# Kernel tuning notes

Hardware: AMD Instinct MI355X
Metric: run time of the kernel (lower is better)

Reference implementation:

```python
import jax, jax.numpy as jnp
import numpy as np

K = 2  # diffusion order
N, S, D, L, C = 4000, 32, 128, 2, 10
THETA = 0.5


def setup_inputs() -> dict:
    key = jax.random.key(0)
    ks = jax.random.split(key, 16)
    w = 0.05  # weight scale to keep tanh/exp in sane range
    return {
        "A": jax.random.uniform(ks[0], (N, N), dtype=jnp.float32),
        "embs": jax.random.normal(ks[1], (L, S, N, D), dtype=jnp.float32),
        "conv1_w": jax.random.normal(ks[2], (K, D, D), dtype=jnp.float32) * w,
        "conv2_w": jax.random.normal(ks[3], (K, D, D), dtype=jnp.float32) * w,
        "lin_in_w": jax.random.normal(ks[4], (D, D), dtype=jnp.float32) * w,
        "lin_out_w": jax.random.normal(ks[5], (D, 2 * D), dtype=jnp.float32) * w,
        "W_psi": jax.random.normal(ks[6], (2 * D, D), dtype=jnp.float32) * w,
        "b_psi": jax.random.normal(ks[7], (D,), dtype=jnp.float32) * w,
        "ae": jax.random.uniform(ks[8], (N, 1, 1), dtype=jnp.float32),
        "ab": jax.random.uniform(ks[9], (N, 1, 1), dtype=jnp.float32),
        "emb_table": jax.random.uniform(ks[10], (N, D), minval=-0.1, maxval=0.1, dtype=jnp.float32),
        "W_p": jax.random.normal(ks[11], (D, C), dtype=jnp.float32) * w,
        "W_c": jax.random.normal(ks[12], (D, D), dtype=jnp.float32) * w,
    }


def _diffusion(A_tilde, X, W):
    # A_tilde: [N,N] (sym-normalized); X: [N,S,D] (linear in X, so batching over S
    # is identical to the per-timestep loop); W: [K,D,D]
    P_f = A_tilde / A_tilde.sum(axis=1, keepdims=True)
    P_v = A_tilde.T / A_tilde.sum(axis=0, keepdims=True)
    Z = jnp.einsum('mn,nsd->msd', P_f, X) @ W[0]
    P_psi_f, P_psi_v = P_f, P_v
    for k in range(1, K):
        if k < K // 2:
            P_psi_f = P_psi_f @ P_f
            M = P_psi_f
        else:
            P_psi_v = P_psi_v @ P_v
            M = P_psi_v
        Z = Z + jnp.einsum('mn,nsd->msd', M, X) @ W[k]
    return Z


def _attention(context, lin_in_w, lin_out_w, ae, ab):
    # context: [N,S,D]; query is the last timestep, output_len == 1
    q = context[:, -1, :] @ lin_in_w.T                    # [N,D]
    scores = jnp.einsum('nd,nsd->ns', q, context)         # [N,S]
    attw = jax.nn.softmax(scores, axis=-1)                # [N,S]
    mix = attw[:, None, :] * context.transpose(0, 2, 1)   # [N,D,S]
    delta_t = jnp.arange(S - 1, -1, -1, dtype=context.dtype)  # flipped arange
    bt = jnp.exp(-ab * delta_t[None, None, :])            # [N,1,S]
    term2 = jax.nn.relu(ae * mix * bt)                    # [N,D,S]
    mix_sum = (term2 + mix).sum(axis=-1)                  # [N,D]
    combined = jnp.concatenate([mix_sum, q], axis=-1)     # [N,2D]
    return jnp.tanh(combined @ lin_out_w.T)               # [N,D]


def reference(A, embs, conv1_w, conv2_w, lin_in_w, lin_out_w, W_psi, b_psi,
              ae, ab, emb_table, W_p, W_c):
    n = A.shape[0]
    A_t = A + jnp.eye(n, dtype=A.dtype)
    d_inv_sqrt = A_t.sum(axis=1) ** -0.5
    A_tilde = d_inv_sqrt[:, None] * A_t * d_inv_sqrt[None, :]

    outs = []
    for l in range(L):
        X = embs[l].transpose(1, 0, 2)                    # [N,S,D]
        h = _diffusion(A_tilde, X, conv1_w)
        h = jax.nn.relu(h)
        h = _diffusion(A_tilde, h, conv2_w)               # [N,S,D]
        # fusion with theta = 0.5 (h_tilde is the raw embedding)
        fused = jnp.concatenate([THETA * h, (1.0 - THETA) * X], axis=-1) @ W_psi + b_psi
        outs.append(_attention(fused, lin_in_w, lin_out_w, ae, ab))
    outputs = jnp.stack(outs)                             # [L,N,D]

    # embedding lookup over arange(N) is an identity gather
    qs = jax.nn.relu(emb_table)                           # [N,D]
    betas = jnp.exp(jnp.einsum('nd,lne->lde', qs, jnp.tanh(outputs)))  # [L,D,D]
    betas = betas / betas.sum(axis=0)
    Z = jnp.einsum('lnd,lde->ne', outputs, betas)         # [N,D]

    P = jax.nn.softmax(Z @ W_p, axis=1)                   # [N,C]
    C_mat = P.T @ Z                                       # [C,D]
    eta = P.T @ A @ P                                     # [C,C] (vectorized eta_ij)
    C_prime = jax.nn.relu(eta @ (C_mat @ W_c.T))          # [C,D]
    return P @ C_prime                                    # [N,D]
```

## Files before the change

### kernel.cpp

```cpp
#include <hip/hip_runtime.h>
#include <hip/hip_bf16.h>


typedef __attribute__((ext_vector_type(8))) short short8;
typedef __attribute__((ext_vector_type(4))) float f32x4;
typedef __attribute__((ext_vector_type(4))) unsigned short us4;

__device__ __forceinline__ unsigned short f2bf(float x) {
  unsigned int u = __builtin_bit_cast(unsigned int, x);
  u += 0x7FFFu + ((u >> 16) & 1u);
  return (unsigned short)(u >> 16);
}

__device__ __forceinline__ void gload16(const void* g, void* l) {
  __builtin_amdgcn_global_load_lds((const __attribute__((address_space(1))) void*)g,
                                   (__attribute__((address_space(3))) void*)l, 16, 0, 0);
}

__device__ __forceinline__ void barrier_() {
  __builtin_amdgcn_sched_barrier(0);
  asm volatile("" ::: "memory");
  __builtin_amdgcn_s_barrier();
  asm volatile("" ::: "memory");
  __builtin_amdgcn_sched_barrier(0);
}

template<int TRANS, int RELU>
__global__ __launch_bounds__(512, 2)
void gemm256(const unsigned short* __restrict__ Ap, int lda,
             const unsigned short* __restrict__ Bp, int ldb,
             unsigned short* __restrict__ outp, int ldo, int K)
{
  __shared__ alignas(16) unsigned short lds[81920];
  const int t = threadIdx.x;
  const int lane = t & 63;
  const int wave = t >> 6;
  const int wm = wave >> 2;
  const int wn = wave & 3;
  const int lrow = lane & 15;
  const int kgrp = lane >> 4;
  const int slotbase = (kgrp ^ (lrow & 7)) << 3;

  const int b = blockIdx.x;
  const int wg = (b & 7) * 32 + (b >> 3);
  const int m0 = (wg >> 4) << 8;
  const int j0 = (wg & 15) << 8;

  const int prow = t >> 3;
  const int lslot = (t & 7) ^ (prow & 7);
  const unsigned short* srcA = Ap + (size_t)(m0 + prow) * lda + lslot * 8;
  const unsigned short* srcB = Bp + (size_t)(j0 + prow) * ldb + lslot * 8;
  const size_t a64 = (size_t)64 * lda, a128 = (size_t)128 * lda;
  const size_t b64 = (size_t)64 * ldb, b128 = (size_t)128 * ldb;
  unsigned short* dA = &lds[t * 8];
  unsigned short* dB = &lds[32768 + t * 8];
  const int NT = K >> 6;

#define STG_A(h, kb, kt) { const unsigned short* s_ = srcA + (h)*a128 + (size_t)(kt)*64; \
    gload16(s_, dA + (kb)*16384 + (h)*8192); \
    gload16(s_ + a64, dA + (kb)*16384 + (h)*8192 + 4096); }
#define STG_B(h, bb, kt) { const unsigned short* s_ = srcB + (h)*b128 + (size_t)(kt)*64; \
    gload16(s_, dB + (bb)*16384 + (h)*8192); \
    gload16(s_ + b64, dB + (bb)*16384 + (h)*8192 + 4096); }

  const int arb = wm * 8192 + lrow * 64 + slotbase;
  const int brb = (wn >> 1) * 8192 + ((wn & 1) << 12) + lrow * 64 + slotbase;

#define RD_A(dst, base_off) \
  _Pragma("unroll") for (int mf_ = 0; mf_ < 4; ++mf_) { \
    dst[mf_][0] = *(const short8*)&lds[(base_off) + mf_*1024]; \
    dst[mf_][1] = *(const short8*)&lds[((base_off) ^ 32) + mf_*1024]; }
#define RD_B(dst, base_off) \
  _Pragma("unroll") for (int nf_ = 0; nf_ < 2; ++nf_) { \
    dst[nf_][0] = *(const short8*)&lds[(base_off) + nf_*1024]; \
    dst[nf_][1] = *(const short8*)&lds[((base_off) ^ 32) + nf_*1024]; }

#define MFMA16(AF, BF, MB, NB) \
  _Pragma("unroll") for (int mf_ = 0; mf_ < 4; ++mf_) \
  _Pragma("unroll") for (int nf_ = 0; nf_ < 2; ++nf_) { \
    acc[(MB)+mf_][(NB)+nf_] = __builtin_amdgcn_mfma_f32_16x16x32_bf16(AF[mf_][0], BF[nf_][0], acc[(MB)+mf_][(NB)+nf_], 0,0,0); \
    acc[(MB)+mf_][(NB)+nf_] = __builtin_amdgcn_mfma_f32_16x16x32_bf16(AF[mf_][1], BF[nf_][1], acc[(MB)+mf_][(NB)+nf_], 0,0,0); }

#define LGKM(n) { asm volatile("s_waitcnt lgkmcnt(" #n ")" ::: "memory"); \
                  __builtin_amdgcn_sched_barrier(0); }

  f32x4 acc[8][4];
#pragma unroll
  for (int i = 0; i < 8; ++i)
#pragma unroll
    for (int j = 0; j < 4; ++j) acc[i][j] = f32x4{0.f, 0.f, 0.f, 0.f};

  short8 a0[4][2], a1[4][2], b0[2][2], b1[2][2];

  STG_B(0, 0, 0); STG_B(1, 0, 0); STG_A(0, 0, 0); STG_A(1, 0, 0);
  STG_B(0, 1, 1); STG_B(1, 1, 1); STG_A(0, 1, 1); STG_A(1, 1, 1);
  asm volatile("s_waitcnt vmcnt(8)" ::: "memory");
  barrier_();
  RD_A(a0, arb);
  RD_B(b0, 32768 + brb);

  int rb3 = 0, rn3 = 1, sb3 = 2;
  for (int V = 0; V < NT; ++V) {
    const int abuf  = (V & 1) << 14;
    const int anbuf = ((V + 1) & 1) << 14;
    const int bbuf  = 32768 + (rb3 << 14);
    const int bnbuf = 32768 + (rn3 << 14);
    const bool stg = (V + 2 < NT);
    const bool rdn = (V + 1 < NT);

    RD_B(b1, bbuf + brb + 2048);
    LGKM(4);
    if (stg) STG_B(0, sb3, V + 2);
    __builtin_amdgcn_s_setprio(1);
    MFMA16(a0, b0, 0, 0);
    __builtin_amdgcn_s_setprio(0);
    barrier_();

    RD_A(a1, abuf + arb + 4096);
    LGKM(8);
    if (stg) STG_B(1, sb3, V + 2);
    __builtin_amdgcn_s_setprio(1);
    MFMA16(a0, b1, 0, 2);
    __builtin_amdgcn_s_setprio(0);
    if (stg) { asm volatile("s_waitcnt vmcnt(4)" ::: "memory"); }
    else     { asm volatile("s_waitcnt vmcnt(0)" ::: "memory"); }
    barrier_();

    if (rdn) { RD_A(a0, anbuf + arb); LGKM(8); }
    else     { LGKM(0); }
    if (stg) STG_A(0, (V & 1), V + 2);
    __builtin_amdgcn_s_setprio(1);
    MFMA16(a1, b0, 4, 0);
    __builtin_amdgcn_s_setprio(0);
    barrier_();

    if (rdn) { RD_B(b0, bnbuf + brb); LGKM(4); }
    else     { LGKM(0); }
    if (stg) STG_A(1, (V & 1), V + 2);
    __builtin_amdgcn_s_setprio(1);
    MFMA16(a1, b1, 4, 2);
    __builtin_amdgcn_s_setprio(0);
    barrier_();

    rb3 = rn3; rn3 = (rn3 == 2) ? 0 : rn3 + 1;
    sb3 = (sb3 == 2) ? 0 : sb3 + 1;
  }

#pragma unroll
  for (int mf = 0; mf < 8; ++mf) {
#pragma unroll
    for (int nf = 0; nf < 4; ++nf) {
      const int m = m0 + wm * 128 + mf * 16 + kgrp * 4;
      const int j = j0 + wn * 64 + nf * 16 + lrow;
      if (TRANS) {
        us4 pk;
#pragma unroll
        for (int r = 0; r < 4; ++r) pk[r] = f2bf(acc[mf][nf][r]);
        *(us4*)(outp + (size_t)j * ldo + m) = pk;
      } else {
#pragma unroll
        for (int r = 0; r < 4; ++r) {
          float v = acc[mf][nf][r];
          if (RELU) v = fmaxf(v, 0.f);
          outp[(size_t)(m + r) * ldo + j] = f2bf(v);
        }
      }
    }
  }
#undef STG_A
#undef STG_B
#undef RD_A
#undef RD_B
#undef MFMA16
#undef LGKM
}

template<int EPI, int RELU, int BIAS>
__global__ __launch_bounds__(256)
void gemm_nt(const unsigned short* __restrict__ A1,
             const unsigned short* __restrict__ A2,
             int k_switch, int a_zstride, int lda,
             const unsigned short* __restrict__ B, int ldb,
             void* __restrict__ outp,
             long o_j, long o_m, long o_z, long o_jt,
             const float* __restrict__ bias, int K)
{
  __shared__ alignas(16) unsigned short At[128*32];
  __shared__ alignas(16) unsigned short Bt[128*32];
  const int t = threadIdx.x;
  const int lane = t & 63;
  const int wave = t >> 6;
  const int m0 = blockIdx.x << 7;
  const int jt = blockIdx.y;
  const int j0 = jt << 7;
  const int z  = blockIdx.z;
  const int wm = (wave >> 1) << 6;
  const int wn = (wave & 1) << 6;
  const int lrow = lane & 15;
  const int kgrp = lane >> 4;

  const unsigned short* A1z = A1 + (long)z * a_zstride;
  const unsigned short* A2z = A2 + (long)z * a_zstride;

  f32x4 acc[4][4];
#pragma unroll
  for (int i = 0; i < 4; ++i)
#pragma unroll
    for (int j = 0; j < 4; ++j) acc[i][j] = f32x4{0.f, 0.f, 0.f, 0.f};

  const int r0 = t >> 2, q0 = t & 3;
  const int c1 = t + 256;
  const int r1 = c1 >> 2, q1 = c1 & 3;

  for (int k0 = 0; k0 < K; k0 += 32) {
    const unsigned short* As; int ka;
    if (k0 < k_switch) { As = A1z; ka = k0; } else { As = A2z; ka = k0 - k_switch; }
    gload16(As + (long)(m0 + r0) * lda + ka + q0 * 8, At + t * 8);
    gload16(As + (long)(m0 + r1) * lda + ka + q1 * 8, At + c1 * 8);
    gload16(B  + (long)(j0 + r0) * ldb + k0 + q0 * 8, Bt + t * 8);
    gload16(B  + (long)(j0 + r1) * ldb + k0 + q1 * 8, Bt + c1 * 8);
    __syncthreads();
    short8 af[4], bv[4];
#pragma unroll
    for (int i = 0; i < 4; ++i)
      af[i] = *(const short8*)(At + (wm + i * 16 + lrow) * 32 + kgrp * 8);
#pragma unroll
    for (int i = 0; i < 4; ++i)
      bv[i] = *(const short8*)(Bt + (wn + i * 16 + lrow) * 32 + kgrp * 8);
#pragma unroll
    for (int i = 0; i < 4; ++i)
#pragma unroll
      for (int j = 0; j < 4; ++j)
        acc[i][j] = __builtin_amdgcn_mfma_f32_16x16x32_bf16(af[i], bv[j], acc[i][j], 0, 0, 0);
    __syncthreads();
  }

  const int mlb = wm + kgrp * 4;
#pragma unroll
  for (int i = 0; i < 4; ++i) {
#pragma unroll
    for (int j = 0; j < 4; ++j) {
      const int jl = wn + j * 16 + lrow;
      const int ml = mlb + i * 16;
      if (EPI == 0) {
        long base = (long)jl * o_j + (long)(m0 + ml) * o_m + (long)z * o_z + (long)jt * o_jt;
        us4 pk;
#pragma unroll
        for (int r = 0; r < 4; ++r) pk[r] = f2bf(acc[i][j][r]);
        *(us4*)((unsigned short*)outp + base) = pk;
      } else {
        float* of = (float*)outp;
        float badd = BIAS ? bias[j0 + jl] : 0.f;
#pragma unroll
        for (int r = 0; r < 4; ++r) {
          long idx = (long)jl * o_j + (long)(m0 + ml + r) * o_m + (long)z * o_z + (long)jt * o_jt;
          of[idx] = acc[i][j][r] + badd;
        }
      }
    }
  }
}

__global__ __launch_bounds__(256) void rowsum_dis(const float* __restrict__ A,
                                                  float* __restrict__ dis) {
  int m = blockIdx.x;
  if (m >= 4000) { if (threadIdx.x == 0) dis[m] = 0.f; return; }
  const float* r = A + (long)m * 4000;
  float a = 0.f;
  for (int i = threadIdx.x; i < 1000; i += 256) {
    float4 v = ((const float4*)r)[i];
    a += v.x + v.y + v.z + v.w;
  }
  for (int o = 32; o; o >>= 1) a += __shfl_xor(a, o);
  __shared__ float ls[4];
  if ((threadIdx.x & 63) == 0) ls[threadIdx.x >> 6] = a;
  __syncthreads();
  if (threadIdx.x == 0) dis[m] = rsqrtf(1.f + ls[0] + ls[1] + ls[2] + ls[3]);
}

__global__ __launch_bounds__(256) void wrow_kernel(const float* __restrict__ A,
                                                   const float* __restrict__ dis,
                                                   float* __restrict__ iwrow) {
  int m = blockIdx.x;
  if (m >= 4000) { if (threadIdx.x == 0) iwrow[m] = 0.f; return; }
  const float* r = A + (long)m * 4000;
  float a = 0.f;
  for (int n = threadIdx.x; n < 4000; n += 256) a += r[n] * dis[n];
  for (int o = 32; o; o >>= 1) a += __shfl_xor(a, o);
  __shared__ float ls[4];
  if ((threadIdx.x & 63) == 0) ls[threadIdx.x >> 6] = a;
  __syncthreads();
  if (threadIdx.x == 0) iwrow[m] = 1.f / (ls[0] + ls[1] + ls[2] + ls[3] + dis[m]);
}

__global__ __launch_bounds__(256) void wcol_part(const float* __restrict__ A,
                                                 const float* __restrict__ dis,
                                                 float* __restrict__ part) {
  int j = blockIdx.x * 256 + threadIdx.x;
  int mz = blockIdx.y;
  float a = 0.f;
  if (j < 4000) {
    int ms = mz * 125;
    for (int m = ms; m < ms + 125; ++m) a += A[(long)m * 4000 + j] * dis[m];
  }
  part[(long)mz * 4096 + j] = a;
}

__global__ __launch_bounds__(256) void wcol_fin(const float* __restrict__ part,
                                                const float* __restrict__ dis,
                                                float* __restrict__ iwcol) {
  int j = blockIdx.x * 256 + threadIdx.x;
  float s = 0.f;
  for (int z = 0; z < 32; ++z) s += part[(long)z * 4096 + j];
  iwcol[j] = (j < 4000) ? 1.f / (s + dis[j]) : 0.f;
}

__global__ __launch_bounds__(256) void build_P(const float* __restrict__ A,
                                               const float* __restrict__ dis,
                                               const float* __restrict__ iwrow,
                                               const float* __restrict__ iwcol,
                                               unsigned short* __restrict__ Pcat,
                                               unsigned short* __restrict__ PV,
                                               unsigned short* __restrict__ PVT) {
  __shared__ float tile[64][65];
  int m0 = blockIdx.y * 64, n0 = blockIdx.x * 64;
#pragma unroll
  for (int i = 0; i < 16; ++i) {
    int idx = i * 256 + threadIdx.x;
    int lr = idx >> 6, lc = idx & 63;
    int m = m0 + lr, n = n0 + lc;
    float v = 0.f;
    if (m < 4000 && n < 4000) {
      float a = A[(long)m * 4000 + n];
      if (m == n) a += 1.f;
      v = a * dis[n];
    }
    Pcat[(long)m * 8192 + n] = f2bf(v * iwrow[m]);
    float pv = v * iwcol[m];
    PVT[(long)m * 4096 + n] = f2bf(pv);
    tile[lr][lc] = pv;
  }
  __syncthreads();
#pragma unroll
  for (int i = 0; i < 16; ++i) {
    int idx = i * 256 + threadIdx.x;
    int lr = idx >> 6, lc = idx & 63;
    PV[(long)(n0 + lr) * 4096 + (m0 + lc)] = f2bf(tile[lc][lr]);
  }
}

__global__ __launch_bounds__(256) void prep_weights(const float* __restrict__ lin_in,
                                                    const float* __restrict__ lin_out,
                                                    const float* __restrict__ c1,
                                                    const float* __restrict__ c2,
                                                    const float* __restrict__ wpsi,
                                                    float* __restrict__ LWiT, float* __restrict__ LWoT,
                                                    unsigned short* __restrict__ CW1T,
                                                    unsigned short* __restrict__ CW2T,
                                                    unsigned short* __restrict__ WPST) {
  int i = blockIdx.x * 256 + threadIdx.x;
  if (i < 16384) {
    int e = i >> 7, d = i & 127;
    LWiT[e * 128 + d] = lin_in[d * 128 + e];
  } else if (i < 49152) {
    int k = i - 16384; int ii = k >> 7, d = k & 127;
    LWoT[k] = lin_out[d * 256 + ii];
  } else if (i < 81920) {
    int k = i - 49152; int j = k >> 7, kk = k & 127;
    CW1T[k] = f2bf(c1[(j >> 7) * 16384 + kk * 128 + (j & 127)]);
  } else if (i < 114688) {
    int k = i - 81920; int j = k >> 7, kk = k & 127;
    CW2T[k] = f2bf(c2[(j >> 7) * 16384 + kk * 128 + (j & 127)]);
  } else if (i < 147456) {
    int k = i - 114688; int e = k >> 8, d2 = k & 255;
    WPST[k] = f2bf(0.5f * wpsi[d2 * 128 + e]);
  }
}

__global__ __launch_bounds__(256) void convert_X(const float* __restrict__ embsL,
                                                 unsigned short* __restrict__ X) {
  long i4 = (long)blockIdx.x * 256 + threadIdx.x;
  long e = i4 << 2;
  int n = (int)(e >> 12);
  int r = (int)(e & 4095);
  us4 o;
  if (n < 4000) {
    int s = r >> 7, d = r & 127;
    float4 v = *(const float4*)(embsL + ((long)s * 4000 + n) * 128 + d);
    o[0] = f2bf(v.x); o[1] = f2bf(v.y); o[2] = f2bf(v.z); o[3] = f2bf(v.w);
  } else { o[0] = o[1] = o[2] = o[3] = 0; }
  *(us4*)(X + (long)n * 4096 + r) = o;
}

__global__ __launch_bounds__(128) void attention_kernel(const float* __restrict__ F,
                                                        const float* __restrict__ LWiT,
                                                        const float* __restrict__ LWoT,
                                                        const float* __restrict__ ae,
                                                        const float* __restrict__ ab,
                                                        float* __restrict__ outp) {
  int n = blockIdx.x, t = threadIdx.x;
  __shared__ float Fs[32 * 132];
  __shared__ float qv[128], msum[128], attw[32], btv[32];
  const float* Fr = F + (long)n * 4096;
  for (int i = t; i < 4096; i += 128) { int s = i >> 7, d = i & 127; Fs[s * 132 + d] = Fr[i]; }
  __syncthreads();
  {
    float a = 0.f;
    const float* Frow = Fs + 31 * 132;
    for (int e = 0; e < 128; ++e) a += Frow[e] * LWiT[e * 128 + t];
    qv[t] = a;
  }
  __syncthreads();
  if (t < 32) {
    float sc = 0.f;
    for (int d = 0; d < 128; ++d) sc += qv[d] * Fs[t * 132 + d];
    float mx = sc;
    for (int o = 16; o; o >>= 1) mx = fmaxf(mx, __shfl_xor(mx, o, 32));
    float ex = expf(sc - mx), sm = ex;
    for (int o = 16; o; o >>= 1) sm += __shfl_xor(sm, o, 32);
    attw[t] = ex / sm;
  } else if (t >= 64 && t < 96) {
    int s = t - 64;
    btv[s] = expf(-ab[n] * (float)(31 - s));
  }
  __syncthreads();
  {
    float aen = ae[n], acc = 0.f;
    for (int s = 0; s < 32; ++s) {
      float f = Fs[s * 132 + t];
      acc += attw[s] * (f + aen * btv[s] * fmaxf(f, 0.f));
    }
    msum[t] = acc;
  }
  __syncthreads();
  {
    float a = 0.f;
    for (int e = 0; e < 128; ++e) a += msum[e] * LWoT[e * 128 + t];
    for (int e = 0; e < 128; ++e) a += qv[e] * LWoT[(e + 128) * 128 + t];
    outp[(long)n * 128 + t] = tanhf(a);
  }
}

__global__ __launch_bounds__(256) void tanh_qs(const float* __restrict__ outs,
                                               const float* __restrict__ embt,
                                               float* __restrict__ T, float* __restrict__ qs) {
  long i = (long)blockIdx.x * 256 + threadIdx.x;
  if (i < 1024000) T[i] = tanhf(outs[i]);
  else { long j = i - 1024000; if (j < 512000) qs[j] = fmaxf(embt[j], 0.f); }
}

__global__ __launch_bounds__(256) void betas_raw_kernel(const float* __restrict__ qs,
                                                        const float* __restrict__ T,
                                                        float* __restrict__ braw) {
  int e = threadIdx.x & 127, dl = threadIdx.x >> 7;
  int d = blockIdx.x * 2 + dl, l = blockIdx.y;
  const float* Tl = T + (long)l * 512000;
  float acc = 0.f;
  for (int n = 0; n < 4000; ++n) acc += qs[(long)n * 128 + d] * Tl[(long)n * 128 + e];
  braw[((long)l * 128 + d) * 128 + e] = acc;
}

__global__ __launch_bounds__(256) void bnorm_kernel(const float* __restrict__ braw,
                                                    float* __restrict__ bn) {
  int i = blockIdx.x * 256 + threadIdx.x;
  float b0 = expf(braw[i]), b1 = expf(braw[16384 + i]);
  float s = b0 + b1;
  bn[i] = b0 / s;
  bn[16384 + i] = b1 / s;
}

__global__ __launch_bounds__(256) void z_kernel(const float* __restrict__ outs,
                                                const float* __restrict__ bn,
                                                float* __restrict__ Zb) {
  int n = blockIdx.x * 2 + (threadIdx.x >> 7);
  int e = threadIdx.x & 127;
  float acc = 0.f;
  for (int l = 0; l < 2; ++l) {
    const float* orow = outs + ((long)l * 4000 + n) * 128;
    const float* brow = bn + (long)l * 16384;
    for (int d = 0; d < 128; ++d) acc += orow[d] * brow[d * 128 + e];
  }
  Zb[(long)n * 128 + e] = acc;
}

__global__ __launch_bounds__(256) void p_kernel(const float* __restrict__ Zb,
                                                const float* __restrict__ Wp,
                                                float* __restrict__ P) {
  int n = blockIdx.x * 4 + (threadIdx.x >> 6);
  int c = threadIdx.x & 63;
  float val = 0.f;
  if (c < 10) {
    const float* zr = Zb + (long)n * 128;
    for (int d = 0; d < 128; ++d) val += zr[d] * Wp[d * 10 + c];
  }
  float mx = val;
  for (int i = 0; i < 10; ++i) mx = fmaxf(mx, __shfl(val, i, 64));
  float ex = (c < 10) ? expf(val - mx) : 0.f;
  float sm = 0.f;
  for (int i = 0; i < 10; ++i) sm += __shfl(ex, i, 64);
  if (c < 12) P[(long)n * 12 + c] = (c < 10) ? ex / sm : 0.f;
}

__global__ __launch_bounds__(256) void ap_kernel(const float* __restrict__ A,
                                                 const float* __restrict__ P,
                                                 float* __restrict__ AP) {
  int m = blockIdx.x, t = threadIdx.x;
  const float* Ar = A + (long)m * 4000;
  float acc[10];
#pragma unroll
  for (int c = 0; c < 10; ++c) acc[c] = 0.f;
  for (int n = t; n < 4000; n += 256) {
    float a = Ar[n];
    const float* Pr = P + (long)n * 12;
#pragma unroll
    for (int c = 0; c < 10; ++c) acc[c] += a * Pr[c];
  }
#pragma unroll
  for (int c = 0; c < 10; ++c)
    for (int o = 32; o; o >>= 1) acc[c] += __shfl_xor(acc[c], o);
  __shared__ float ls[4][10];
  if ((t & 63) == 0)
    for (int c = 0; c < 10; ++c) ls[t >> 6][c] = acc[c];
  __syncthreads();
  if (t < 10) AP[(long)m * 12 + t] = ls[0][t] + ls[1][t] + ls[2][t] + ls[3][t];
  if (t >= 10 && t < 12) AP[(long)m * 12 + t] = 0.f;
}

__global__ __launch_bounds__(256) void etacm_part(const float* __restrict__ P,
                                                  const float* __restrict__ AP,
                                                  const float* __restrict__ Z,
                                                  float* __restrict__ peta,
                                                  float* __restrict__ pcm) {
  int b = blockIdx.x, t = threadIdx.x;
  int ms = b * 63, me = ms + 63; if (me > 4000) me = 4000;
  int i_ = t / 10, j_ = t % 10;
  float ea = 0.f;
  float ca[5];
#pragma unroll
  for (int k = 0; k < 5; ++k) ca[k] = 0.f;
  for (int m = ms; m < me; ++m) {
    if (t < 100) ea += P[(long)m * 12 + i_] * AP[(long)m * 12 + j_];
#pragma unroll
    for (int k = 0; k < 5; ++k) {
      int idx = t + 256 * k;
      int c = idx >> 7, e = idx & 127;
      ca[k] += P[(long)m * 12 + c] * Z[(long)m * 128 + e];
    }
  }
  if (t < 100) peta[(long)b * 100 + t] = ea;
#pragma unroll
  for (int k = 0; k < 5; ++k) pcm[(long)b * 1280 + t + 256 * k] = ca[k];
}

__global__ __launch_bounds__(256) void final_small(const float* __restrict__ peta,
                                                   const float* __restrict__ pcm,
                                                   const float* __restrict__ Wc,
                                                   float* __restrict__ cprime) {
  __shared__ float eta_s[100], cm_s[1280], tmp_s[1280];
  int t = threadIdx.x;
  if (t < 100) {
    float s = 0.f;
    for (int b = 0; b < 64; ++b) s += peta[(long)b * 100 + t];
    eta_s[t] = s;
  }
  for (int i = t; i < 1280; i += 256) {
    float s = 0.f;
    for (int b = 0; b < 64; ++b) s += pcm[(long)b * 1280 + i];
    cm_s[i] = s;
  }
  __syncthreads();
  for (int i = t; i < 1280; i += 256) {
    int c = i >> 7, d = i & 127;
    float s = 0.f;
    for (int e = 0; e < 128; ++e) s += cm_s[c * 128 + e] * Wc[d * 128 + e];
    tmp_s[i] = s;
  }
  __syncthreads();
  for (int i = t; i < 1280; i += 256) {
    int c = i >> 7, d = i & 127;
    float s = 0.f;
    for (int j = 0; j < 10; ++j) s += eta_s[c * 10 + j] * tmp_s[j * 128 + d];
    cprime[i] = fmaxf(s, 0.f);
  }
}

__global__ __launch_bounds__(256) void out_kernel(const float* __restrict__ P,
                                                  const float* __restrict__ cpr,
                                                  float* __restrict__ out) {
  int idx = blockIdx.x * 256 + threadIdx.x;
  int n = idx >> 7, d = idx & 127;
  float s = 0.f;
#pragma unroll
  for (int c = 0; c < 10; ++c) s += P[(long)n * 12 + c] * cpr[c * 128 + d];
  out[idx] = s;
}

extern "C" void kernel_launch(void* const* d_in, const int* in_sizes, int n_in,
                              void* d_out, int out_size, void* d_ws, size_t ws_size,
                              hipStream_t stream) {
  (void)in_sizes; (void)n_in; (void)out_size; (void)ws_size;
  const float* A      = (const float*)d_in[0];
  const float* embs   = (const float*)d_in[1];
  const float* conv1w = (const float*)d_in[2];
  const float* conv2w = (const float*)d_in[3];
  const float* lin_in = (const float*)d_in[4];
  const float* lin_out= (const float*)d_in[5];
  const float* Wpsi   = (const float*)d_in[6];
  const float* bpsi   = (const float*)d_in[7];
  const float* ae     = (const float*)d_in[8];
  const float* ab     = (const float*)d_in[9];
  const float* embt   = (const float*)d_in[10];
  const float* Wp     = (const float*)d_in[11];
  const float* Wc     = (const float*)d_in[12];
  float* out = (float*)d_out;
  char* ws = (char*)d_ws;

  size_t off = 0;
  auto alloc = [&](size_t b) { size_t r = off; off += (b + 255) & ~(size_t)255; return r; };
  unsigned short* PCAT = (unsigned short*)(ws + alloc((size_t)4096 * 8192 * 2));
  char*           BTF  = ws + alloc((size_t)4096 * 8192 * 2);
  unsigned short* BT   = (unsigned short*)BTF;
  float*          Ff   = (float*)BTF;
  unsigned short* XBF  = (unsigned short*)(ws + alloc((size_t)4096 * 4096 * 2));
  unsigned short* PV   = XBF;
  unsigned short* HBUF = (unsigned short*)(ws + alloc((size_t)4096 * 4096 * 2));
  unsigned short* PVT  = HBUF;
  float* DIS   = (float*)(ws + alloc(4096 * 4));
  float* IWROW = (float*)(ws + alloc(4096 * 4));
  float* IWCOL = (float*)(ws + alloc(4096 * 4));
  float* WCP   = (float*)(ws + alloc((size_t)32 * 4096 * 4));
  float* LWIT  = (float*)(ws + alloc(16384 * 4));
  float* LWOT  = (float*)(ws + alloc(32768 * 4));
  unsigned short* CW1T = (unsigned short*)(ws + alloc(32768 * 2));
  unsigned short* CW2T = (unsigned short*)(ws + alloc(32768 * 2));
  unsigned short* WPST = (unsigned short*)(ws + alloc(32768 * 2));
  float* OUTS = (float*)(ws + alloc((size_t)2 * 4000 * 128 * 4));
  float* TT   = (float*)(ws + alloc((size_t)2 * 4000 * 128 * 4));
  float* QS   = (float*)(ws + alloc((size_t)4000 * 128 * 4));
  float* BRAW = (float*)(ws + alloc(32768 * 4));
  float* BNRM = (float*)(ws + alloc(32768 * 4));
  float* ZB   = (float*)(ws + alloc((size_t)4000 * 128 * 4));
  float* PP   = (float*)(ws + alloc((size_t)4000 * 12 * 4));
  float* APB  = (float*)(ws + alloc((size_t)4000 * 12 * 4));
  float* PETA = (float*)(ws + alloc((size_t)64 * 100 * 4));
  float* PCM  = (float*)(ws + alloc((size_t)64 * 1280 * 4));
  float* CPR  = (float*)(ws + alloc(1280 * 4));

  const int BIG = 1 << 30;

  rowsum_dis<<<4096, 256, 0, stream>>>(A, DIS);
  wrow_kernel<<<4096, 256, 0, stream>>>(A, DIS, IWROW);
  wcol_part<<<dim3(16, 32), 256, 0, stream>>>(A, DIS, WCP);
  wcol_fin<<<16, 256, 0, stream>>>(WCP, DIS, IWCOL);
  prep_weights<<<576, 256, 0, stream>>>(lin_in, lin_out, conv1w, conv2w, Wpsi,
                                        LWIT, LWOT, CW1T, CW2T, WPST);
  build_P<<<dim3(64, 64), 256, 0, stream>>>(A, DIS, IWROW, IWCOL, PCAT, PV, PVT);

  gemm256<1, 0><<<256, 512, 0, stream>>>(PVT, 4096, PV, 4096, PCAT + 4096, 8192, 4096);

  for (int l = 0; l < 2; ++l) {
    convert_X<<<16384, 256, 0, stream>>>(embs + (long)l * 32 * 4000 * 128, XBF);
    gemm_nt<0, 0, 0><<<dim3(32, 2, 32), 256, 0, stream>>>(
        XBF, XBF, BIG, 128, 4096, CW1T, 128,
        BT, 8192L, 1L, 128L * 8192, 4096L, nullptr, 128);
    gemm256<0, 1><<<256, 512, 0, stream>>>(PCAT, 8192, BT, 8192, HBUF, 4096, 8192);
    gemm_nt<0, 0, 0><<<dim3(32, 2, 32), 256, 0, stream>>>(
        HBUF, HBUF, BIG, 128, 4096, CW2T, 128,
        BT, 8192L, 1L, 128L * 8192, 4096L, nullptr, 128);
    gemm256<0, 0><<<256, 512, 0, stream>>>(PCAT, 8192, BT, 8192, HBUF, 4096, 8192);
    gemm_nt<2, 0, 1><<<dim3(32, 1, 32), 256, 0, stream>>>(
        HBUF, XBF, 128, 128, 4096, WPST, 256,
        Ff, 1L, 4096L, 128L, 0L, bpsi, 256);
    attention_kernel<<<4000, 128, 0, stream>>>(Ff, LWIT, LWOT, ae, ab,
                                               OUTS + (long)l * 512000);
  }

  tanh_qs<<<6000, 256, 0, stream>>>(OUTS, embt, TT, QS);
  betas_raw_kernel<<<dim3(64, 2), 256, 0, stream>>>(QS, TT, BRAW);
  bnorm_kernel<<<64, 256, 0, stream>>>(BRAW, BNRM);
  z_kernel<<<2000, 256, 0, stream>>>(OUTS, BNRM, ZB);
  p_kernel<<<1000, 256, 0, stream>>>(ZB, Wp, PP);
  ap_kernel<<<4000, 256, 0, stream>>>(A, PP, APB);
  etacm_part<<<64, 256, 0, stream>>>(PP, APB, ZB, PETA, PCM);
  final_small<<<1, 256, 0, stream>>>(PETA, PCM, Wc, CPR);
  out_kernel<<<2000, 256, 0, stream>>>(PP, CPR, out);
}
```

Measured before the change: 1.544 ms.

## Fold query projection into fused GEMM, batch attention output GEMM, split betas reduction

```diff
diff --git a/kernel.cpp b/kernel.cpp
--- a/kernel.cpp
+++ b/kernel.cpp
@@ -10,6 +10,10 @@
   unsigned int u = __builtin_bit_cast(unsigned int, x);
   u += 0x7FFFu + ((u >> 16) & 1u);
   return (unsigned short)(u >> 16);
+}
+__device__ __forceinline__ float bf2f(unsigned short u) {
+  unsigned int x = ((unsigned int)u) << 16;
+  return __builtin_bit_cast(float, x);
 }
 
 __device__ __forceinline__ void gload16(const void* g, void* l) {
@@ -175,18 +179,18 @@
 #undef LGKM
 }
 
-template<int EPI, int RELU, int BIAS>
-__global__ __launch_bounds__(256)
-void gemm_nt(const unsigned short* __restrict__ A1,
-             const unsigned short* __restrict__ A2,
-             int k_switch, int a_zstride, int lda,
-             const unsigned short* __restrict__ B, int ldb,
-             void* __restrict__ outp,
-             long o_j, long o_m, long o_z, long o_jt,
-             const float* __restrict__ bias, int K)
+template<int EPI, int KFULL, int MINB>
+__global__ __launch_bounds__(256, MINB)
+void gemm_smallk(const unsigned short* __restrict__ A1,
+                 const unsigned short* __restrict__ A2,
+                 int k_switch, int a_zstride, int lda,
+                 const unsigned short* __restrict__ B, int ldb,
+                 void* __restrict__ outp,
+                 long o_j, long o_m, long o_z, long o_jt,
+                 const float* __restrict__ bias)
 {
-  __shared__ alignas(16) unsigned short At[128*32];
-  __shared__ alignas(16) unsigned short Bt[128*32];
+  __shared__ alignas(16) unsigned short At[(KFULL / 32) * 4096];
+  __shared__ alignas(16) unsigned short Bt[(KFULL / 32) * 4096];
   const int t = threadIdx.x;
   const int lane = t & 63;
   const int wave = t >> 6;
@@ -202,37 +206,42 @@
   const unsigned short* A1z = A1 + (long)z * a_zstride;
   const unsigned short* A2z = A2 + (long)z * a_zstride;
 
-  f32x4 acc[4][4];
-#pragma unroll
-  for (int i = 0; i < 4; ++i)
-#pragma unroll
-    for (int j = 0; j < 4; ++j) acc[i][j] = f32x4{0.f, 0.f, 0.f, 0.f};
-
   const int r0 = t >> 2, q0 = t & 3;
   const int c1 = t + 256;
   const int r1 = c1 >> 2, q1 = c1 & 3;
 
-  for (int k0 = 0; k0 < K; k0 += 32) {
+#pragma unroll
+  for (int kk = 0; kk < KFULL / 32; ++kk) {
+    const int k0 = kk * 32;
     const unsigned short* As; int ka;
     if (k0 < k_switch) { As = A1z; ka = k0; } else { As = A2z; ka = k0 - k_switch; }
-    gload16(As + (long)(m0 + r0) * lda + ka + q0 * 8, At + t * 8);
-    gload16(As + (long)(m0 + r1) * lda + ka + q1 * 8, At + c1 * 8);
-    gload16(B  + (long)(j0 + r0) * ldb + k0 + q0 * 8, Bt + t * 8);
-    gload16(B  + (long)(j0 + r1) * ldb + k0 + q1 * 8, Bt + c1 * 8);
-    __syncthreads();
+    gload16(As + (long)(m0 + r0) * lda + ka + q0 * 8, At + kk * 4096 + t * 8);
+    gload16(As + (long)(m0 + r1) * lda + ka + q1 * 8, At + kk * 4096 + c1 * 8);
+    gload16(B  + (long)(j0 + r0) * ldb + k0 + q0 * 8, Bt + kk * 4096 + t * 8);
+    gload16(B  + (long)(j0 + r1) * ldb + k0 + q1 * 8, Bt + kk * 4096 + c1 * 8);
+  }
+  __syncthreads();
+
+  f32x4 acc[4][4];
+#pragma unroll
+  for (int i = 0; i < 4; ++i)
+#pragma unroll
+    for (int j = 0; j < 4; ++j) acc[i][j] = f32x4{0.f, 0.f, 0.f, 0.f};
+
+#pragma unroll
+  for (int kk = 0; kk < KFULL / 32; ++kk) {
     short8 af[4], bv[4];
 #pragma unroll
     for (int i = 0; i < 4; ++i)
-      af[i] = *(const short8*)(At + (wm + i * 16 + lrow) * 32 + kgrp * 8);
+      af[i] = *(const short8*)(At + kk * 4096 + (wm + i * 16 + lrow) * 32 + kgrp * 8);
 #pragma unroll
     for (int i = 0; i < 4; ++i)
-      bv[i] = *(const short8*)(Bt + (wn + i * 16 + lrow) * 32 + kgrp * 8);
+      bv[i] = *(const short8*)(Bt + kk * 4096 + (wn + i * 16 + lrow) * 32 + kgrp * 8);
 #pragma unroll
     for (int i = 0; i < 4; ++i)
 #pragma unroll
       for (int j = 0; j < 4; ++j)
         acc[i][j] = __builtin_amdgcn_mfma_f32_16x16x32_bf16(af[i], bv[j], acc[i][j], 0, 0, 0);
-    __syncthreads();
   }
 
   const int mlb = wm + kgrp * 4;
@@ -248,13 +257,22 @@
 #pragma unroll
         for (int r = 0; r < 4; ++r) pk[r] = f2bf(acc[i][j][r]);
         *(us4*)((unsigned short*)outp + base) = pk;
-      } else {
+      } else if (EPI == 2) {
         float* of = (float*)outp;
-        float badd = BIAS ? bias[j0 + jl] : 0.f;
+        float badd = bias[j0 + jl];
 #pragma unroll
         for (int r = 0; r < 4; ++r) {
           long idx = (long)jl * o_j + (long)(m0 + ml + r) * o_m + (long)z * o_z + (long)jt * o_jt;
           of[idx] = acc[i][j][r] + badd;
+        }
+      } else {
+        float* of = (float*)outp;
+#pragma unroll
+        for (int r = 0; r < 4; ++r) {
+          int mm = m0 + ml + r;
+          int n = mm & 4095, l = mm >> 12;
+          if (n < 4000)
+            of[(size_t)l * 512000 + (size_t)n * 128 + (j0 + jl)] = tanhf(acc[i][j][r]);
         }
       }
     }
@@ -349,31 +367,47 @@
   }
 }
 
-__global__ __launch_bounds__(256) void prep_weights(const float* __restrict__ lin_in,
-                                                    const float* __restrict__ lin_out,
+__global__ __launch_bounds__(256) void prep_weights(const float* __restrict__ lin_out,
                                                     const float* __restrict__ c1,
                                                     const float* __restrict__ c2,
                                                     const float* __restrict__ wpsi,
-                                                    float* __restrict__ LWiT, float* __restrict__ LWoT,
                                                     unsigned short* __restrict__ CW1T,
                                                     unsigned short* __restrict__ CW2T,
-                                                    unsigned short* __restrict__ WPST) {
+                                                    unsigned short* __restrict__ WPST,
+                                                    unsigned short* __restrict__ LWOB) {
   int i = blockIdx.x * 256 + threadIdx.x;
-  if (i < 16384) {
-    int e = i >> 7, d = i & 127;
-    LWiT[e * 128 + d] = lin_in[d * 128 + e];
-  } else if (i < 49152) {
-    int k = i - 16384; int ii = k >> 7, d = k & 127;
-    LWoT[k] = lin_out[d * 256 + ii];
-  } else if (i < 81920) {
-    int k = i - 49152; int j = k >> 7, kk = k & 127;
-    CW1T[k] = f2bf(c1[(j >> 7) * 16384 + kk * 128 + (j & 127)]);
-  } else if (i < 114688) {
-    int k = i - 81920; int j = k >> 7, kk = k & 127;
+  if (i < 32768) {
+    int j = i >> 7, kk = i & 127;
+    CW1T[i] = f2bf(c1[(j >> 7) * 16384 + kk * 128 + (j & 127)]);
+  } else if (i < 65536) {
+    int k = i - 32768; int j = k >> 7, kk = k & 127;
     CW2T[k] = f2bf(c2[(j >> 7) * 16384 + kk * 128 + (j & 127)]);
-  } else if (i < 147456) {
-    int k = i - 114688; int e = k >> 8, d2 = k & 255;
+  } else if (i < 98304) {
+    int k = i - 65536; int e = k >> 8, d2 = k & 255;
     WPST[k] = f2bf(0.5f * wpsi[d2 * 128 + e]);
+  } else if (i < 131072) {
+    int k = i - 98304;
+    LWOB[k] = f2bf(lin_out[k]);
+  }
+}
+
+__global__ __launch_bounds__(256) void wq_prep(const float* __restrict__ lin_in,
+                                               const float* __restrict__ bpsi,
+                                               const unsigned short* __restrict__ WPST,
+                                               unsigned short* __restrict__ WQ,
+                                               float* __restrict__ BQ) {
+  int b = blockIdx.x, t = threadIdx.x;
+  if (b < 128) {
+    int idx = b * 256 + t;
+    int d = idx >> 8, k2 = idx & 255;
+    float acc = 0.f;
+    for (int e = 0; e < 128; ++e)
+      acc += lin_in[d * 128 + e] * bf2f(WPST[e * 256 + k2]);
+    WQ[idx] = f2bf(acc);
+  } else if (t < 128) {
+    float acc = 0.f;
+    for (int e = 0; e < 128; ++e) acc += bpsi[e] * lin_in[t * 128 + e];
+    BQ[t] = acc;
   }
 }
 
@@ -392,24 +426,22 @@
   *(us4*)(X + (long)n * 4096 + r) = o;
 }
 
-__global__ __launch_bounds__(128) void attention_kernel(const float* __restrict__ F,
-                                                        const float* __restrict__ LWiT,
-                                                        const float* __restrict__ LWoT,
-                                                        const float* __restrict__ ae,
-                                                        const float* __restrict__ ab,
-                                                        float* __restrict__ outp) {
+__global__ __launch_bounds__(128) void attention2(const float* __restrict__ F,
+                                                  const float* __restrict__ Q,
+                                                  const float* __restrict__ ae,
+                                                  const float* __restrict__ ab,
+                                                  unsigned short* __restrict__ CATl) {
   int n = blockIdx.x, t = threadIdx.x;
+  if (n >= 4000) {
+    CATl[(size_t)n * 256 + t] = 0;
+    CATl[(size_t)n * 256 + 128 + t] = 0;
+    return;
+  }
   __shared__ float Fs[32 * 132];
-  __shared__ float qv[128], msum[128], attw[32], btv[32];
+  __shared__ float qv[128], attw[32], btv[32];
   const float* Fr = F + (long)n * 4096;
   for (int i = t; i < 4096; i += 128) { int s = i >> 7, d = i & 127; Fs[s * 132 + d] = Fr[i]; }
-  __syncthreads();
-  {
-    float a = 0.f;
-    const float* Frow = Fs + 31 * 132;
-    for (int e = 0; e < 128; ++e) a += Frow[e] * LWiT[e * 128 + t];
-    qv[t] = a;
-  }
+  qv[t] = Q[(long)n * 128 + t];
   __syncthreads();
   if (t < 32) {
     float sc = 0.f;
@@ -424,21 +456,13 @@
     btv[s] = expf(-ab[n] * (float)(31 - s));
   }
   __syncthreads();
-  {
-    float aen = ae[n], acc = 0.f;
-    for (int s = 0; s < 32; ++s) {
-      float f = Fs[s * 132 + t];
-      acc += attw[s] * (f + aen * btv[s] * fmaxf(f, 0.f));
-    }
-    msum[t] = acc;
-  }
-  __syncthreads();
-  {
-    float a = 0.f;
-    for (int e = 0; e < 128; ++e) a += msum[e] * LWoT[e * 128 + t];
-    for (int e = 0; e < 128; ++e) a += qv[e] * LWoT[(e + 128) * 128 + t];
-    outp[(long)n * 128 + t] = tanhf(a);
-  }
+  float aen = ae[n], acc = 0.f;
+  for (int s = 0; s < 32; ++s) {
+    float f = Fs[s * 132 + t];
+    acc += attw[s] * (f + aen * btv[s] * fmaxf(f, 0.f));
+  }
+  CATl[(size_t)n * 256 + t] = f2bf(acc);
+  CATl[(size_t)n * 256 + 128 + t] = f2bf(qv[t]);
 }
 
 __global__ __launch_bounds__(256) void tanh_qs(const float* __restrict__ outs,
@@ -449,21 +473,28 @@
   else { long j = i - 1024000; if (j < 512000) qs[j] = fmaxf(embt[j], 0.f); }
 }
 
-__global__ __launch_bounds__(256) void betas_raw_kernel(const float* __restrict__ qs,
-                                                        const float* __restrict__ T,
-                                                        float* __restrict__ braw) {
+__global__ __launch_bounds__(256) void betas_part(const float* __restrict__ qs,
+                                                  const float* __restrict__ T,
+                                                  float* __restrict__ out) {
   int e = threadIdx.x & 127, dl = threadIdx.x >> 7;
-  int d = blockIdx.x * 2 + dl, l = blockIdx.y;
+  int d = blockIdx.x * 2 + dl, l = blockIdx.y, nc = blockIdx.z;
   const float* Tl = T + (long)l * 512000;
   float acc = 0.f;
-  for (int n = 0; n < 4000; ++n) acc += qs[(long)n * 128 + d] * Tl[(long)n * 128 + e];
-  braw[((long)l * 128 + d) * 128 + e] = acc;
-}
-
-__global__ __launch_bounds__(256) void bnorm_kernel(const float* __restrict__ braw,
+  int n0 = nc * 500;
+  for (int n = n0; n < n0 + 500; ++n)
+    acc += qs[(long)n * 128 + d] * Tl[(long)n * 128 + e];
+  out[(long)nc * 32768 + (long)l * 16384 + d * 128 + e] = acc;
+}
+
+__global__ __launch_bounds__(256) void bnorm_kernel(const float* __restrict__ brawp,
                                                     float* __restrict__ bn) {
   int i = blockIdx.x * 256 + threadIdx.x;
-  float b0 = expf(braw[i]), b1 = expf(braw[16384 + i]);
+  float s0 = 0.f, s1 = 0.f;
+  for (int nc = 0; nc < 8; ++nc) {
+    s0 += brawp[(long)nc * 32768 + i];
+    s1 += brawp[(long)nc * 32768 + 16384 + i];
+  }
+  float b0 = expf(s0), b1 = expf(s1);
   float s = b0 + b1;
   bn[i] = b0 / s;
   bn[16384 + i] = b1 / s;
@@ -629,15 +660,18 @@
   float* IWROW = (float*)(ws + alloc(4096 * 4));
   float* IWCOL = (float*)(ws + alloc(4096 * 4));
   float* WCP   = (float*)(ws + alloc((size_t)32 * 4096 * 4));
-  float* LWIT  = (float*)(ws + alloc(16384 * 4));
-  float* LWOT  = (float*)(ws + alloc(32768 * 4));
   unsigned short* CW1T = (unsigned short*)(ws + alloc(32768 * 2));
   unsigned short* CW2T = (unsigned short*)(ws + alloc(32768 * 2));
   unsigned short* WPST = (unsigned short*)(ws + alloc(32768 * 2));
+  unsigned short* LWOB = (unsigned short*)(ws + alloc(32768 * 2));
+  unsigned short* WQ   = (unsigned short*)(ws + alloc(32768 * 2));
+  float* BQ    = (float*)(ws + alloc(128 * 4));
+  float* QBUF  = (float*)(ws + alloc((size_t)4096 * 128 * 4));
+  unsigned short* CAT = (unsigned short*)(ws + alloc((size_t)8192 * 256 * 2));
   float* OUTS = (float*)(ws + alloc((size_t)2 * 4000 * 128 * 4));
   float* TT   = (float*)(ws + alloc((size_t)2 * 4000 * 128 * 4));
   float* QS   = (float*)(ws + alloc((size_t)4000 * 128 * 4));
-  float* BRAW = (float*)(ws + alloc(32768 * 4));
+  float* BRAWP= (float*)(ws + alloc((size_t)8 * 32768 * 4));
   float* BNRM = (float*)(ws + alloc(32768 * 4));
   float* ZB   = (float*)(ws + alloc((size_t)4000 * 128 * 4));
   float* PP   = (float*)(ws + alloc((size_t)4000 * 12 * 4));
@@ -652,32 +686,39 @@
   wrow_kernel<<<4096, 256, 0, stream>>>(A, DIS, IWROW);
   wcol_part<<<dim3(16, 32), 256, 0, stream>>>(A, DIS, WCP);
   wcol_fin<<<16, 256, 0, stream>>>(WCP, DIS, IWCOL);
-  prep_weights<<<576, 256, 0, stream>>>(lin_in, lin_out, conv1w, conv2w, Wpsi,
-                                        LWIT, LWOT, CW1T, CW2T, WPST);
+  prep_weights<<<512, 256, 0, stream>>>(lin_out, conv1w, conv2w, Wpsi,
+                                        CW1T, CW2T, WPST, LWOB);
+  wq_prep<<<129, 256, 0, stream>>>(lin_in, bpsi, WPST, WQ, BQ);
   build_P<<<dim3(64, 64), 256, 0, stream>>>(A, DIS, IWROW, IWCOL, PCAT, PV, PVT);
 
   gemm256<1, 0><<<256, 512, 0, stream>>>(PVT, 4096, PV, 4096, PCAT + 4096, 8192, 4096);
 
   for (int l = 0; l < 2; ++l) {
     convert_X<<<16384, 256, 0, stream>>>(embs + (long)l * 32 * 4000 * 128, XBF);
-    gemm_nt<0, 0, 0><<<dim3(32, 2, 32), 256, 0, stream>>>(
+    gemm_smallk<0, 128, 2><<<dim3(32, 2, 32), 256, 0, stream>>>(
         XBF, XBF, BIG, 128, 4096, CW1T, 128,
-        BT, 8192L, 1L, 128L * 8192, 4096L, nullptr, 128);
+        BT, 8192L, 1L, 128L * 8192, 4096L, nullptr);
     gemm256<0, 1><<<256, 512, 0, stream>>>(PCAT, 8192, BT, 8192, HBUF, 4096, 8192);
-    gemm_nt<0, 0, 0><<<dim3(32, 2, 32), 256, 0, stream>>>(
+    gemm_smallk<0, 128, 2><<<dim3(32, 2, 32), 256, 0, stream>>>(
         HBUF, HBUF, BIG, 128, 4096, CW2T, 128,
-        BT, 8192L, 1L, 128L * 8192, 4096L, nullptr, 128);
+        BT, 8192L, 1L, 128L * 8192, 4096L, nullptr);
     gemm256<0, 0><<<256, 512, 0, stream>>>(PCAT, 8192, BT, 8192, HBUF, 4096, 8192);
-    gemm_nt<2, 0, 1><<<dim3(32, 1, 32), 256, 0, stream>>>(
+    gemm_smallk<2, 256, 1><<<dim3(32, 1, 32), 256, 0, stream>>>(
         HBUF, XBF, 128, 128, 4096, WPST, 256,
-        Ff, 1L, 4096L, 128L, 0L, bpsi, 256);
-    attention_kernel<<<4000, 128, 0, stream>>>(Ff, LWIT, LWOT, ae, ab,
-                                               OUTS + (long)l * 512000);
-  }
+        Ff, 1L, 4096L, 128L, 0L, bpsi);
+    gemm_smallk<2, 256, 1><<<dim3(32, 1, 1), 256, 0, stream>>>(
+        HBUF + 31 * 128, XBF + 31 * 128, 128, 0, 4096, WQ, 256,
+        QBUF, 1L, 128L, 0L, 0L, BQ);
+    attention2<<<4096, 128, 0, stream>>>(Ff, QBUF, ae, ab, CAT + (size_t)l * 4096 * 256);
+  }
+
+  gemm_smallk<3, 256, 1><<<dim3(64, 1, 1), 256, 0, stream>>>(
+      CAT, CAT, BIG, 0, 256, LWOB, 256,
+      OUTS, 0L, 0L, 0L, 0L, nullptr);
 
   tanh_qs<<<6000, 256, 0, stream>>>(OUTS, embt, TT, QS);
-  betas_raw_kernel<<<dim3(64, 2), 256, 0, stream>>>(QS, TT, BRAW);
-  bnorm_kernel<<<64, 256, 0, stream>>>(BRAW, BNRM);
+  betas_part<<<dim3(64, 2, 8), 256, 0, stream>>>(QS, TT, BRAWP);
+  bnorm_kernel<<<64, 256, 0, stream>>>(BRAWP, BNRM);
   z_kernel<<<2000, 256, 0, stream>>>(OUTS, BNRM, ZB);
   p_kernel<<<1000, 256, 0, stream>>>(ZB, Wp, PP);
   ap_kernel<<<4000, 256, 0, stream>>>(A, PP, APB);
```

New measurement: 1.544 ms (median of 2 runs). No clear change (+0.0%).
